# Optimization experiments

Hardware: AMD Instinct MI355X
Metric: run time of the kernel (lower is better)

Reference implementation:

```python
import jax, jax.numpy as jnp
import numpy as np

N_NODES = 50000
N_EDGES = 800000
D_FEAT = 128
D_HID = 128
N_CLASSES = 16


def setup_inputs() -> dict:
    key = jax.random.key(0)
    ks = jax.random.split(key, 5)
    x = jax.random.normal(ks[0], (N_NODES, D_FEAT), dtype=jnp.float32)
    edge_index = jax.random.randint(ks[1], (2, N_EDGES), 0, N_NODES, dtype=jnp.int32)
    # Glorot-ish scaled weights to keep activations in a sane range
    W1 = jax.random.normal(ks[2], (D_FEAT, D_HID), dtype=jnp.float32) * 0.05
    b1 = jnp.zeros((D_HID,), dtype=jnp.float32)
    W2 = jax.random.normal(ks[3], (D_HID, N_CLASSES), dtype=jnp.float32) * 0.05
    b2 = jnp.zeros((N_CLASSES,), dtype=jnp.float32)
    return {"x": x, "edge_index": edge_index, "W1": W1, "b1": b1, "W2": W2, "b2": b2}


def _gcn_conv(h, src, dst, norm, W, b, num_nodes):
    # linear transform first (F_in >= F_out ordering as in PyG GCNConv)
    h = h @ W                              # [N, F_out]
    msg = h[src] * norm[:, None]           # gather + edge-wise scale  [E+N, F_out]
    out = jax.ops.segment_sum(msg, dst, num_segments=num_nodes)  # scatter-add
    return out + b


def reference(x, edge_index, W1, b1, W2, b2):
    n = x.shape[0]
    loop = jnp.arange(n, dtype=edge_index.dtype)
    src = jnp.concatenate([edge_index[0], loop])  # add self-loops
    dst = jnp.concatenate([edge_index[1], loop])
    # symmetric normalization: deg^{-1/2}[src] * deg^{-1/2}[dst]
    deg = jax.ops.segment_sum(jnp.ones_like(dst, dtype=x.dtype), dst, num_segments=n)
    dis = jax.lax.rsqrt(jnp.maximum(deg, 1.0))  # deg >= 1 thanks to self-loops
    norm = dis[src] * dis[dst]
    h = jax.nn.relu(_gcn_conv(x, src, dst, norm, W1, b1, n))
    # dropout is identity in eval mode
    out = _gcn_conv(h, src, dst, norm, W2, b2, n)
    return jax.nn.sigmoid(out)
```

## Files before the change

### kernel.cpp

```cpp
#include <hip/hip_runtime.h>
#include <math.h>

#define NN 50000
#define NE 800000
#define DF 128
#define NC 16
#define WLD 136
#define NBIN 196
#define EPB 2048
#define HB ((NE + EPB - 1) / EPB)
#define HL (NBIN * HB)
#define PB ((HL + 255) / 256)
#define GB ((NN + 63) / 64)

typedef __bf16 bf16x8 __attribute__((ext_vector_type(8)));
typedef __bf16 bf16x4 __attribute__((ext_vector_type(4)));
typedef float  f32x4  __attribute__((ext_vector_type(4)));

__global__ void k_prep(const float* __restrict__ W1, const float* __restrict__ W2,
                       __bf16* __restrict__ W1T, __bf16* __restrict__ W2T) {
    int i = blockIdx.x * blockDim.x + threadIdx.x;
    if (i < DF * DF) {
        int n = i >> 7, k = i & 127;
        W1T[i] = (__bf16)W1[k * DF + n];
    }
    int j = i - DF * DF;
    if (j >= 0 && j < NC * DF) {
        int n = j >> 7, k = j & 127;
        W2T[j] = (__bf16)W2[k * NC + n];
    }
}

__global__ __launch_bounds__(256) void k_gemm1_hist(const float* __restrict__ X,
                                                    const __bf16* __restrict__ W1T,
                                                    __bf16* __restrict__ H1,
                                                    const int* __restrict__ dst,
                                                    int* __restrict__ h) {
    __shared__ __bf16 wlds[DF * WLD];
    __shared__ int hc[NBIN];
    if (blockIdx.x >= GB) {
        const int bb = blockIdx.x - GB;
        const int t = threadIdx.x;
        if (t < NBIN) hc[t] = 0;
        __syncthreads();
        const int base = bb * EPB;
#pragma unroll
        for (int i = 0; i < EPB / 256; ++i) {
            int e = base + i * 256 + t;
            if (e < NE) atomicAdd(&hc[dst[e] >> 8], 1);
        }
        __syncthreads();
        if (t < NBIN) h[t * HB + bb] = hc[t];
        return;
    }
    const int wid = threadIdx.x >> 6, lane = threadIdx.x & 63;
    const int m0 = blockIdx.x * 64 + wid * 16;
    const int m = m0 + (lane & 15);
    const int mc = (m < NN) ? m : NN - 1;
    const int l15 = lane & 15;
    const int kb = (lane >> 4) * 8;

    float4 xf[8];
#pragma unroll
    for (int q = 0; q < 4; ++q) {
        xf[2 * q]     = *(const float4*)&X[(size_t)mc * DF + q * 32 + kb];
        xf[2 * q + 1] = *(const float4*)&X[(size_t)mc * DF + q * 32 + kb + 4];
    }
    for (int i = threadIdx.x; i < DF * 16; i += 256) {
        int row = i >> 4, c8 = i & 15;
        *(bf16x8*)&wlds[row * WLD + c8 * 8] = ((const bf16x8*)W1T)[i];
    }
    __syncthreads();

    f32x4 acc[8];
#pragma unroll
    for (int nf = 0; nf < 8; ++nf) acc[nf] = (f32x4){0.f, 0.f, 0.f, 0.f};
#pragma unroll
    for (int ks = 0; ks < 4; ++ks) {
        float4 x0 = xf[2 * ks], x1 = xf[2 * ks + 1];
        bf16x8 xa;
        xa[0] = (__bf16)x0.x; xa[1] = (__bf16)x0.y; xa[2] = (__bf16)x0.z; xa[3] = (__bf16)x0.w;
        xa[4] = (__bf16)x1.x; xa[5] = (__bf16)x1.y; xa[6] = (__bf16)x1.z; xa[7] = (__bf16)x1.w;
#pragma unroll
        for (int nf = 0; nf < 8; ++nf) {
            bf16x8 wa = *(const bf16x8*)&wlds[(nf * 16 + l15) * WLD + ks * 32 + kb];
            acc[nf] = __builtin_amdgcn_mfma_f32_16x16x32_bf16(wa, xa, acc[nf], 0, 0, 0);
        }
    }
    if (m < NN) {
#pragma unroll
        for (int nf = 0; nf < 8; ++nf) {
            bf16x4 o;
            o[0] = (__bf16)acc[nf][0]; o[1] = (__bf16)acc[nf][1];
            o[2] = (__bf16)acc[nf][2]; o[3] = (__bf16)acc[nf][3];
            *(bf16x4*)&H1[(size_t)m * DF + nf * 16 + (lane >> 4) * 4] = o;
        }
    }
}

__global__ __launch_bounds__(256) void k_hpart(const int* __restrict__ h,
                                               int* __restrict__ part) {
    __shared__ int ws[4];
    const int b = blockIdx.x, t = threadIdx.x;
    const int idx = b * 256 + t;
    int s = (idx < HL) ? h[idx] : 0;
    for (int o = 32; o > 0; o >>= 1) s += __shfl_down(s, o);
    if ((t & 63) == 0) ws[t >> 6] = s;
    __syncthreads();
    if (t == 0) part[b] = ws[0] + ws[1] + ws[2] + ws[3];
}

__global__ __launch_bounds__(512) void k_hscan_part(const int* __restrict__ part,
                                                    int* __restrict__ partoff,
                                                    int* __restrict__ hscan) {
    __shared__ int s[512];
    const int t = threadIdx.x;
    int v = (t < PB) ? part[t] : 0;
    s[t] = v;
    __syncthreads();
    for (int o = 1; o < 512; o <<= 1) {
        int x = (t >= o) ? s[t - o] : 0;
        __syncthreads();
        s[t] += x;
        __syncthreads();
    }
    if (t < PB) partoff[t] = s[t] - v;
    if (t == 511) hscan[HL] = s[511];
}

__global__ __launch_bounds__(256) void k_hoff(const int* __restrict__ h,
                                              const int* __restrict__ partoff,
                                              int* __restrict__ hscan) {
    __shared__ int s[256];
    const int b = blockIdx.x, t = threadIdx.x;
    const int idx = b * 256 + t;
    int v = (idx < HL) ? h[idx] : 0;
    s[t] = v;
    __syncthreads();
    for (int o = 1; o < 256; o <<= 1) {
        int x = (t >= o) ? s[t - o] : 0;
        __syncthreads();
        s[t] += x;
        __syncthreads();
    }
    if (idx < HL) hscan[idx] = partoff[b] + s[t] - v;
}

__global__ __launch_bounds__(256) void k_scatterA(const int* __restrict__ src,
                                                  const int* __restrict__ dst,
                                                  const int* __restrict__ hscan,
                                                  int* __restrict__ ebuf) {
    __shared__ int cur[NBIN];
    const int bb = blockIdx.x, t = threadIdx.x;
    if (t < NBIN) cur[t] = hscan[t * HB + bb];
    __syncthreads();
    const int base = bb * EPB;
#pragma unroll
    for (int i = 0; i < EPB / 256; ++i) {
        int e = base + i * 256 + t;
        if (e < NE) {
            int s = src[e], d = dst[e];
            int pos = atomicAdd(&cur[d >> 8], 1);
            ebuf[pos] = s | ((d & 255) << 16);
        }
    }
}

__global__ __launch_bounds__(256) void k_rankB(const int* __restrict__ ebuf,
                                               const int* __restrict__ hscan,
                                               int* __restrict__ off,
                                               float* __restrict__ dis,
                                               unsigned short* __restrict__ rec) {
    __shared__ int cnt[256], s[256], cur[256];
    const int bin = blockIdx.x, t = threadIdx.x;
    const int base = hscan[bin * HB];
    const int end  = hscan[(bin + 1) * HB];
    cnt[t] = 0;
    __syncthreads();
    for (int e = base + t; e < end; e += 256)
        atomicAdd(&cnt[(ebuf[e] >> 16) & 255], 1);
    __syncthreads();
    int c = cnt[t];
    s[t] = c;
    __syncthreads();
    for (int o = 1; o < 256; o <<= 1) {
        int x = (t >= o) ? s[t - o] : 0;
        __syncthreads();
        s[t] += x;
        __syncthreads();
    }
    int lo = s[t] - c;
    int d = (bin << 8) + t;
    if (d < NN) {
        off[d] = base + lo;
        dis[d] = rsqrtf((float)(c + 1));
    }
    if (bin == NBIN - 1 && t == 0) off[NN] = NE;
    cur[t] = base + lo;
    __syncthreads();
    for (int e = base + t; e < end; e += 256) {
        int ed = ebuf[e];
        int p = atomicAdd(&cur[(ed >> 16) & 255], 1);
        rec[p] = (unsigned short)(ed & 0xFFFF);
    }
}

__global__ __launch_bounds__(256) void k_agg1g2(const __bf16* __restrict__ H1,
                                                const float* __restrict__ dis,
                                                const float* __restrict__ b1,
                                                const __bf16* __restrict__ W2T,
                                                const int* __restrict__ off,
                                                const unsigned short* __restrict__ rec,
                                                float* __restrict__ H2) {
    const int wid = threadIdx.x >> 6, lane = threadIdx.x & 63;
    const int n = blockIdx.x * 4 + wid;
    if (n >= NN) return;
    const int g = lane >> 4, l16 = lane & 15;
    const int fo = l16 * 8;
    const float dn = dis[n];

    float a[8];
#pragma unroll
    for (int i = 0; i < 8; ++i) a[i] = 0.f;

    const int e0 = off[n], e1 = off[n + 1];
    int e = e0 + g;
    for (; e + 12 < e1; e += 16) {
        int r0 = rec[e];
        int r1 = rec[e + 4];
        int r2 = rec[e + 8];
        int r3 = rec[e + 12];
        float w0 = dis[r0], w1 = dis[r1], w2 = dis[r2], w3 = dis[r3];
        bf16x8 h0 = *(const bf16x8*)&H1[(size_t)r0 * DF + fo];
        bf16x8 h1 = *(const bf16x8*)&H1[(size_t)r1 * DF + fo];
        bf16x8 h2 = *(const bf16x8*)&H1[(size_t)r2 * DF + fo];
        bf16x8 h3 = *(const bf16x8*)&H1[(size_t)r3 * DF + fo];
#pragma unroll
        for (int i = 0; i < 8; ++i) a[i] += (float)h0[i] * w0;
#pragma unroll
        for (int i = 0; i < 8; ++i) a[i] += (float)h1[i] * w1;
#pragma unroll
        for (int i = 0; i < 8; ++i) a[i] += (float)h2[i] * w2;
#pragma unroll
        for (int i = 0; i < 8; ++i) a[i] += (float)h3[i] * w3;
    }
    for (; e < e1; e += 4) {
        int r = rec[e];
        float w = dis[r];
        bf16x8 h = *(const bf16x8*)&H1[(size_t)r * DF + fo];
#pragma unroll
        for (int i = 0; i < 8; ++i) a[i] += (float)h[i] * w;
    }
#pragma unroll
    for (int i = 0; i < 8; ++i) {
        a[i] += __shfl_xor(a[i], 16);
        a[i] += __shfl_xor(a[i], 32);
    }
    {
        const float d2 = dn * dn;
        float4 b0 = *(const float4*)&b1[fo];
        float4 b4 = *(const float4*)&b1[fo + 4];
        bf16x8 hs = *(const bf16x8*)&H1[(size_t)n * DF + fo];
        a[0] = fmaxf(a[0] * dn + (float)hs[0] * d2 + b0.x, 0.f);
        a[1] = fmaxf(a[1] * dn + (float)hs[1] * d2 + b0.y, 0.f);
        a[2] = fmaxf(a[2] * dn + (float)hs[2] * d2 + b0.z, 0.f);
        a[3] = fmaxf(a[3] * dn + (float)hs[3] * d2 + b0.w, 0.f);
        a[4] = fmaxf(a[4] * dn + (float)hs[4] * d2 + b4.x, 0.f);
        a[5] = fmaxf(a[5] * dn + (float)hs[5] * d2 + b4.y, 0.f);
        a[6] = fmaxf(a[6] * dn + (float)hs[6] * d2 + b4.z, 0.f);
        a[7] = fmaxf(a[7] * dn + (float)hs[7] * d2 + b4.w, 0.f);
    }

    float p[4];
#pragma unroll
    for (int j = 0; j < 4; ++j) {
        bf16x8 wr = *(const bf16x8*)&W2T[(size_t)(g * 4 + j) * DF + fo];
        float s = 0.f;
#pragma unroll
        for (int i = 0; i < 8; ++i) s += a[i] * (float)wr[i];
        p[j] = s;
    }
#pragma unroll
    for (int o = 1; o <= 8; o <<= 1) {
#pragma unroll
        for (int j = 0; j < 4; ++j) p[j] += __shfl_xor(p[j], o);
    }
    if (l16 == 0) {
        f32x4 o4 = {p[0], p[1], p[2], p[3]};
        *(f32x4*)&H2[(size_t)n * NC + g * 4] = o4;
    }
}

__global__ __launch_bounds__(256) void k_agg2(const float* __restrict__ H2,
                                              const float* __restrict__ dis,
                                              const float* __restrict__ b2,
                                              const int* __restrict__ off,
                                              const unsigned short* __restrict__ rec,
                                              float* __restrict__ OUT) {
    const int wid = threadIdx.x >> 6, lane = threadIdx.x & 63;
    const int n = blockIdx.x * 4 + wid;
    if (n >= NN) return;
    const float dn = dis[n];

    const int g = lane >> 3, l8 = lane & 7;
    float ax = 0.f, ay = 0.f;
    const int e0 = off[n], e1 = off[n + 1];
    int e = e0 + g;
    for (; e + 8 < e1; e += 16) {
        int r0 = rec[e];
        int r1 = rec[e + 8];
        float w0 = dis[r0], w1 = dis[r1];
        float2 h0 = *(const float2*)&H2[(size_t)r0 * NC + l8 * 2];
        float2 h1 = *(const float2*)&H2[(size_t)r1 * NC + l8 * 2];
        ax += h0.x * w0;
        ay += h0.y * w0;
        ax += h1.x * w1;
        ay += h1.y * w1;
    }
    for (; e < e1; e += 8) {
        int r = rec[e];
        float w = dis[r];
        float2 h = *(const float2*)&H2[(size_t)r * NC + l8 * 2];
        ax += h.x * w;
        ay += h.y * w;
    }
    ax += __shfl_xor(ax, 8);  ay += __shfl_xor(ay, 8);
    ax += __shfl_xor(ax, 16); ay += __shfl_xor(ay, 16);
    ax += __shfl_xor(ax, 32); ay += __shfl_xor(ay, 32);
    if (g == 0) {
        float d2 = dn * dn;
        float2 hs = *(const float2*)&H2[(size_t)n * NC + l8 * 2];
        float2 bb = *(const float2*)&b2[l8 * 2];
        float vx = ax * dn + hs.x * d2 + bb.x;
        float vy = ay * dn + hs.y * d2 + bb.y;
        float2 o = { 1.0f / (1.0f + expf(-vx)), 1.0f / (1.0f + expf(-vy)) };
        *(float2*)&OUT[(size_t)n * NC + l8 * 2] = o;
    }
}

extern "C" void kernel_launch(void* const* d_in, const int* in_sizes, int n_in,
                              void* d_out, int out_size, void* d_ws, size_t ws_size,
                              hipStream_t stream) {
    const float* X  = (const float*)d_in[0];
    const int*   EI = (const int*)d_in[1];
    const float* W1 = (const float*)d_in[2];
    const float* b1 = (const float*)d_in[3];
    const float* W2 = (const float*)d_in[4];
    const float* b2 = (const float*)d_in[5];
    float* OUT = (float*)d_out;

    const int* src = EI;
    const int* dst = EI + NE;

    char* ws = (char*)d_ws;
    int*    h       = (int*)(ws);
    int*    hscan   = (int*)(ws + 327680);
    int*    hpart   = (int*)(ws + 655360);
    int*    hpartoff= (int*)(ws + 659456);
    int*    off     = (int*)(ws + 663552);
    float*  dis     = (float*)(ws + 868352);
    __bf16* W1T     = (__bf16*)(ws + 1073152);
    __bf16* W2T     = (__bf16*)(ws + 1105920);
    int*    ebuf    = (int*)(ws + 1110016);
    unsigned short* rec = (unsigned short*)(ws + 4310016);
    __bf16* H1      = (__bf16*)(ws + 5910016);
    float*  H2      = (float*)(ws + 18710016);

    const int B = 256;

    k_prep<<<(DF * DF + NC * DF + B - 1) / B, B, 0, stream>>>(W1, W2, W1T, W2T);
    k_gemm1_hist<<<GB + HB, B, 0, stream>>>(X, W1T, H1, dst, h);
    k_hpart<<<PB, B, 0, stream>>>(h, hpart);
    k_hscan_part<<<1, 512, 0, stream>>>(hpart, hpartoff, hscan);
    k_hoff<<<PB, B, 0, stream>>>(h, hpartoff, hscan);
    k_scatterA<<<HB, B, 0, stream>>>(src, dst, hscan, ebuf);
    k_rankB<<<NBIN, B, 0, stream>>>(ebuf, hscan, off, dis, rec);

    k_agg1g2<<<(NN + 3) / 4, B, 0, stream>>>(H1, dis, b1, W2T, off, rec, H2);
    k_agg2<<<(NN + 3) / 4, B, 0, stream>>>(H2, dis, b2, off, rec, OUT);
}
```

Measured before the change: 104.5 us.

## Slice H1 into feature-column slabs and split aggregation into sliced gather plus finalize

H1 is stored as 8 feature slabs of 16 columns each (1.6MB per slab), so the layer-1 gather runs one slab per block and its working set stays cache-resident. The fused agg1+GEMM2 kernel is split into k_aggS, which gathers and writes bf16 partial aggregates per slab, and k_fin, which applies the self-loop, bias, ReLU and W2 projection. The histogram edge-block size is also raised to shrink the scan. Each edge index is now read 8 times, and an extra intermediate buffer plus an extra launch are added.

Measured after the change: 195.6 us. 87.1% more time.

```diff
diff --git a/kernel.cpp b/kernel.cpp
--- a/kernel.cpp
+++ b/kernel.cpp
@@ -5,9 +5,11 @@
 #define NE 800000
 #define DF 128
 #define NC 16
+#define NSL 8
+#define SW 16
 #define WLD 136
 #define NBIN 196
-#define EPB 2048
+#define EPB 8192
 #define HB ((NE + EPB - 1) / EPB)
 #define HL (NBIN * HB)
 #define PB ((HL + 255) / 256)
@@ -33,7 +35,7 @@
 
 __global__ __launch_bounds__(256) void k_gemm1_hist(const float* __restrict__ X,
                                                     const __bf16* __restrict__ W1T,
-                                                    __bf16* __restrict__ H1,
+                                                    __bf16* __restrict__ H1s,
                                                     const int* __restrict__ dst,
                                                     int* __restrict__ h) {
     __shared__ __bf16 wlds[DF * WLD];
@@ -93,7 +95,7 @@
             bf16x4 o;
             o[0] = (__bf16)acc[nf][0]; o[1] = (__bf16)acc[nf][1];
             o[2] = (__bf16)acc[nf][2]; o[3] = (__bf16)acc[nf][3];
-            *(bf16x4*)&H1[(size_t)m * DF + nf * 16 + (lane >> 4) * 4] = o;
+            *(bf16x4*)&H1s[(size_t)nf * NN * SW + (size_t)m * SW + (lane >> 4) * 4] = o;
         }
     }
 }
@@ -110,22 +112,22 @@
     if (t == 0) part[b] = ws[0] + ws[1] + ws[2] + ws[3];
 }
 
-__global__ __launch_bounds__(512) void k_hscan_part(const int* __restrict__ part,
+__global__ __launch_bounds__(256) void k_hscan_part(const int* __restrict__ part,
                                                     int* __restrict__ partoff,
                                                     int* __restrict__ hscan) {
-    __shared__ int s[512];
+    __shared__ int s[256];
     const int t = threadIdx.x;
     int v = (t < PB) ? part[t] : 0;
     s[t] = v;
     __syncthreads();
-    for (int o = 1; o < 512; o <<= 1) {
+    for (int o = 1; o < 256; o <<= 1) {
         int x = (t >= o) ? s[t - o] : 0;
         __syncthreads();
         s[t] += x;
         __syncthreads();
     }
     if (t < PB) partoff[t] = s[t] - v;
-    if (t == 511) hscan[HL] = s[511];
+    if (t == 255) hscan[HL] = s[255];
 }
 
 __global__ __launch_bounds__(256) void k_hoff(const int* __restrict__ h,
@@ -205,80 +207,82 @@
     }
 }
 
-__global__ __launch_bounds__(256) void k_agg1g2(const __bf16* __restrict__ H1,
-                                                const float* __restrict__ dis,
-                                                const float* __restrict__ b1,
-                                                const __bf16* __restrict__ W2T,
-                                                const int* __restrict__ off,
-                                                const unsigned short* __restrict__ rec,
-                                                float* __restrict__ H2) {
+__global__ __launch_bounds__(256) void k_aggS(const __bf16* __restrict__ H1s,
+                                              const float* __restrict__ dis,
+                                              const int* __restrict__ off,
+                                              const unsigned short* __restrict__ rec,
+                                              __bf16* __restrict__ AGGs) {
+    const int s = blockIdx.x & (NSL - 1);
+    const int chunk = blockIdx.x >> 3;
+    const int wid = threadIdx.x >> 6, lane = threadIdx.x & 63;
+    const int n = chunk * 4 + wid;
+    const int eg = lane >> 2;
+    const int fl = lane & 3;
+    const __bf16* Hs = H1s + (size_t)s * NN * SW;
+
+    float a[4] = {0.f, 0.f, 0.f, 0.f};
+    const int e0 = off[n], e1 = off[n + 1];
+    for (int eb = e0; eb < e1; eb += 16) {
+        int e = eb + eg;
+        bool ok = e < e1;
+        int r = rec[ok ? e : eb];
+        float w = ok ? dis[r] : 0.f;
+        bf16x4 hv = *(const bf16x4*)&Hs[(size_t)r * SW + fl * 4];
+#pragma unroll
+        for (int i = 0; i < 4; ++i) a[i] += (float)hv[i] * w;
+    }
+#pragma unroll
+    for (int i = 0; i < 4; ++i) {
+        a[i] += __shfl_xor(a[i], 4);
+        a[i] += __shfl_xor(a[i], 8);
+        a[i] += __shfl_xor(a[i], 16);
+        a[i] += __shfl_xor(a[i], 32);
+    }
+    if (lane < 4) {
+        bf16x4 o;
+        o[0] = (__bf16)a[0]; o[1] = (__bf16)a[1];
+        o[2] = (__bf16)a[2]; o[3] = (__bf16)a[3];
+        *(bf16x4*)&AGGs[(size_t)s * NN * SW + (size_t)n * SW + fl * 4] = o;
+    }
+}
+
+__global__ __launch_bounds__(256) void k_fin(const __bf16* __restrict__ H1s,
+                                             const __bf16* __restrict__ AGGs,
+                                             const float* __restrict__ dis,
+                                             const float* __restrict__ b1,
+                                             const __bf16* __restrict__ W2T,
+                                             float* __restrict__ H2) {
     const int wid = threadIdx.x >> 6, lane = threadIdx.x & 63;
     const int n = blockIdx.x * 4 + wid;
     if (n >= NN) return;
     const int g = lane >> 4, l16 = lane & 15;
     const int fo = l16 * 8;
-    const float dn = dis[n];
+    const float dn = dis[n], d2 = dn * dn;
+    const size_t soff = (size_t)(l16 >> 1) * NN * SW + (size_t)n * SW + (l16 & 1) * 8;
+
+    bf16x8 ag = *(const bf16x8*)&AGGs[soff];
+    bf16x8 hs = *(const bf16x8*)&H1s[soff];
+    float4 b0 = *(const float4*)&b1[fo];
+    float4 b4 = *(const float4*)&b1[fo + 4];
 
     float a[8];
-#pragma unroll
-    for (int i = 0; i < 8; ++i) a[i] = 0.f;
-
-    const int e0 = off[n], e1 = off[n + 1];
-    int e = e0 + g;
-    for (; e + 12 < e1; e += 16) {
-        int r0 = rec[e];
-        int r1 = rec[e + 4];
-        int r2 = rec[e + 8];
-        int r3 = rec[e + 12];
-        float w0 = dis[r0], w1 = dis[r1], w2 = dis[r2], w3 = dis[r3];
-        bf16x8 h0 = *(const bf16x8*)&H1[(size_t)r0 * DF + fo];
-        bf16x8 h1 = *(const bf16x8*)&H1[(size_t)r1 * DF + fo];
-        bf16x8 h2 = *(const bf16x8*)&H1[(size_t)r2 * DF + fo];
-        bf16x8 h3 = *(const bf16x8*)&H1[(size_t)r3 * DF + fo];
-#pragma unroll
-        for (int i = 0; i < 8; ++i) a[i] += (float)h0[i] * w0;
-#pragma unroll
-        for (int i = 0; i < 8; ++i) a[i] += (float)h1[i] * w1;
-#pragma unroll
-        for (int i = 0; i < 8; ++i) a[i] += (float)h2[i] * w2;
-#pragma unroll
-        for (int i = 0; i < 8; ++i) a[i] += (float)h3[i] * w3;
-    }
-    for (; e < e1; e += 4) {
-        int r = rec[e];
-        float w = dis[r];
-        bf16x8 h = *(const bf16x8*)&H1[(size_t)r * DF + fo];
-#pragma unroll
-        for (int i = 0; i < 8; ++i) a[i] += (float)h[i] * w;
-    }
-#pragma unroll
-    for (int i = 0; i < 8; ++i) {
-        a[i] += __shfl_xor(a[i], 16);
-        a[i] += __shfl_xor(a[i], 32);
-    }
-    {
-        const float d2 = dn * dn;
-        float4 b0 = *(const float4*)&b1[fo];
-        float4 b4 = *(const float4*)&b1[fo + 4];
-        bf16x8 hs = *(const bf16x8*)&H1[(size_t)n * DF + fo];
-        a[0] = fmaxf(a[0] * dn + (float)hs[0] * d2 + b0.x, 0.f);
-        a[1] = fmaxf(a[1] * dn + (float)hs[1] * d2 + b0.y, 0.f);
-        a[2] = fmaxf(a[2] * dn + (float)hs[2] * d2 + b0.z, 0.f);
-        a[3] = fmaxf(a[3] * dn + (float)hs[3] * d2 + b0.w, 0.f);
-        a[4] = fmaxf(a[4] * dn + (float)hs[4] * d2 + b4.x, 0.f);
-        a[5] = fmaxf(a[5] * dn + (float)hs[5] * d2 + b4.y, 0.f);
-        a[6] = fmaxf(a[6] * dn + (float)hs[6] * d2 + b4.z, 0.f);
-        a[7] = fmaxf(a[7] * dn + (float)hs[7] * d2 + b4.w, 0.f);
-    }
+    a[0] = fmaxf((float)ag[0] * dn + (float)hs[0] * d2 + b0.x, 0.f);
+    a[1] = fmaxf((float)ag[1] * dn + (float)hs[1] * d2 + b0.y, 0.f);
+    a[2] = fmaxf((float)ag[2] * dn + (float)hs[2] * d2 + b0.z, 0.f);
+    a[3] = fmaxf((float)ag[3] * dn + (float)hs[3] * d2 + b0.w, 0.f);
+    a[4] = fmaxf((float)ag[4] * dn + (float)hs[4] * d2 + b4.x, 0.f);
+    a[5] = fmaxf((float)ag[5] * dn + (float)hs[5] * d2 + b4.y, 0.f);
+    a[6] = fmaxf((float)ag[6] * dn + (float)hs[6] * d2 + b4.z, 0.f);
+    a[7] = fmaxf((float)ag[7] * dn + (float)hs[7] * d2 + b4.w, 0.f);
 
     float p[4];
 #pragma unroll
     for (int j = 0; j < 4; ++j) {
         bf16x8 wr = *(const bf16x8*)&W2T[(size_t)(g * 4 + j) * DF + fo];
-        float s = 0.f;
-#pragma unroll
-        for (int i = 0; i < 8; ++i) s += a[i] * (float)wr[i];
-        p[j] = s;
+        float sum = 0.f;
+#pragma unroll
+        for (int i = 0; i < 8; ++i) sum += a[i] * (float)wr[i];
+        p[j] = sum;
     }
 #pragma unroll
     for (int o = 1; o <= 8; o <<= 1) {
@@ -354,28 +358,30 @@
 
     char* ws = (char*)d_ws;
     int*    h       = (int*)(ws);
-    int*    hscan   = (int*)(ws + 327680);
-    int*    hpart   = (int*)(ws + 655360);
-    int*    hpartoff= (int*)(ws + 659456);
-    int*    off     = (int*)(ws + 663552);
-    float*  dis     = (float*)(ws + 868352);
-    __bf16* W1T     = (__bf16*)(ws + 1073152);
-    __bf16* W2T     = (__bf16*)(ws + 1105920);
-    int*    ebuf    = (int*)(ws + 1110016);
-    unsigned short* rec = (unsigned short*)(ws + 4310016);
-    __bf16* H1      = (__bf16*)(ws + 5910016);
-    float*  H2      = (float*)(ws + 18710016);
+    int*    hscan   = (int*)(ws + 81920);
+    int*    hpart   = (int*)(ws + 163840);
+    int*    hpartoff= (int*)(ws + 167936);
+    int*    off     = (int*)(ws + 172032);
+    float*  dis     = (float*)(ws + 376832);
+    __bf16* W1T     = (__bf16*)(ws + 581632);
+    __bf16* W2T     = (__bf16*)(ws + 614400);
+    int*    ebuf    = (int*)(ws + 622592);
+    unsigned short* rec = (unsigned short*)(ws + 3822592);
+    __bf16* H1s     = (__bf16*)(ws + 5422592);
+    __bf16* AGGs    = (__bf16*)(ws + 18222592);
+    float*  H2      = (float*)(ws + 31022592);
 
     const int B = 256;
 
     k_prep<<<(DF * DF + NC * DF + B - 1) / B, B, 0, stream>>>(W1, W2, W1T, W2T);
-    k_gemm1_hist<<<GB + HB, B, 0, stream>>>(X, W1T, H1, dst, h);
+    k_gemm1_hist<<<GB + HB, B, 0, stream>>>(X, W1T, H1s, dst, h);
     k_hpart<<<PB, B, 0, stream>>>(h, hpart);
-    k_hscan_part<<<1, 512, 0, stream>>>(hpart, hpartoff, hscan);
+    k_hscan_part<<<1, B, 0, stream>>>(hpart, hpartoff, hscan);
     k_hoff<<<PB, B, 0, stream>>>(h, hpartoff, hscan);
     k_scatterA<<<HB, B, 0, stream>>>(src, dst, hscan, ebuf);
     k_rankB<<<NBIN, B, 0, stream>>>(ebuf, hscan, off, dis, rec);
 
-    k_agg1g2<<<(NN + 3) / 4, B, 0, stream>>>(H1, dis, b1, W2T, off, rec, H2);
+    k_aggS<<<NSL * (NN / 4), B, 0, stream>>>(H1s, dis, off, rec, AGGs);
+    k_fin<<<(NN + 3) / 4, B, 0, stream>>>(H1s, AGGs, dis, b1, W2T, H2);
     k_agg2<<<(NN + 3) / 4, B, 0, stream>>>(H2, dis, b2, off, rec, OUT);
 }
```

## Fuse GEMM1 with edge scatter, drop weight prep kernel, shrink bins

Applied to the files above, without the earlier changes.

Removes the separate weight-transpose kernel by having each GEMM block convert W1 to bf16 and transpose it into LDS itself, and by having agg1g2 read W2 directly in fp32. The GEMM is moved out of the histogram kernel and co-scheduled with the edge scatter pass. Histogram bins are narrowed to 128 nodes (391 bins) and edges per block raised to 8192, which shrinks the histogram/scan arrays and lets the scan run in one 256-thread block. In exchange, every GEMM block now does its own uncoalesced transposed LDS writes of W1 from fp32, and rankB leaves half its threads idle per bin.

New measurement: 138.1 us. 32.1% more time.

```diff
diff --git a/kernel.cpp b/kernel.cpp
--- a/kernel.cpp
+++ b/kernel.cpp
@@ -6,8 +6,8 @@
 #define DF 128
 #define NC 16
 #define WLD 136
-#define NBIN 196
-#define EPB 2048
+#define NBIN 391
+#define EPB 8192
 #define HB ((NE + EPB - 1) / EPB)
 #define HL (NBIN * HB)
 #define PB ((HL + 255) / 256)
@@ -17,85 +17,20 @@
 typedef __bf16 bf16x4 __attribute__((ext_vector_type(4)));
 typedef float  f32x4  __attribute__((ext_vector_type(4)));
 
-__global__ void k_prep(const float* __restrict__ W1, const float* __restrict__ W2,
-                       __bf16* __restrict__ W1T, __bf16* __restrict__ W2T) {
-    int i = blockIdx.x * blockDim.x + threadIdx.x;
-    if (i < DF * DF) {
-        int n = i >> 7, k = i & 127;
-        W1T[i] = (__bf16)W1[k * DF + n];
-    }
-    int j = i - DF * DF;
-    if (j >= 0 && j < NC * DF) {
-        int n = j >> 7, k = j & 127;
-        W2T[j] = (__bf16)W2[k * NC + n];
-    }
-}
-
-__global__ __launch_bounds__(256) void k_gemm1_hist(const float* __restrict__ X,
-                                                    const __bf16* __restrict__ W1T,
-                                                    __bf16* __restrict__ H1,
-                                                    const int* __restrict__ dst,
-                                                    int* __restrict__ h) {
-    __shared__ __bf16 wlds[DF * WLD];
+__global__ __launch_bounds__(256) void k_hist(const int* __restrict__ dst,
+                                              int* __restrict__ h) {
     __shared__ int hc[NBIN];
-    if (blockIdx.x >= GB) {
-        const int bb = blockIdx.x - GB;
-        const int t = threadIdx.x;
-        if (t < NBIN) hc[t] = 0;
-        __syncthreads();
-        const int base = bb * EPB;
-#pragma unroll
-        for (int i = 0; i < EPB / 256; ++i) {
-            int e = base + i * 256 + t;
-            if (e < NE) atomicAdd(&hc[dst[e] >> 8], 1);
-        }
-        __syncthreads();
-        if (t < NBIN) h[t * HB + bb] = hc[t];
-        return;
-    }
-    const int wid = threadIdx.x >> 6, lane = threadIdx.x & 63;
-    const int m0 = blockIdx.x * 64 + wid * 16;
-    const int m = m0 + (lane & 15);
-    const int mc = (m < NN) ? m : NN - 1;
-    const int l15 = lane & 15;
-    const int kb = (lane >> 4) * 8;
-
-    float4 xf[8];
-#pragma unroll
-    for (int q = 0; q < 4; ++q) {
-        xf[2 * q]     = *(const float4*)&X[(size_t)mc * DF + q * 32 + kb];
-        xf[2 * q + 1] = *(const float4*)&X[(size_t)mc * DF + q * 32 + kb + 4];
-    }
-    for (int i = threadIdx.x; i < DF * 16; i += 256) {
-        int row = i >> 4, c8 = i & 15;
-        *(bf16x8*)&wlds[row * WLD + c8 * 8] = ((const bf16x8*)W1T)[i];
-    }
-    __syncthreads();
-
-    f32x4 acc[8];
-#pragma unroll
-    for (int nf = 0; nf < 8; ++nf) acc[nf] = (f32x4){0.f, 0.f, 0.f, 0.f};
-#pragma unroll
-    for (int ks = 0; ks < 4; ++ks) {
-        float4 x0 = xf[2 * ks], x1 = xf[2 * ks + 1];
-        bf16x8 xa;
-        xa[0] = (__bf16)x0.x; xa[1] = (__bf16)x0.y; xa[2] = (__bf16)x0.z; xa[3] = (__bf16)x0.w;
-        xa[4] = (__bf16)x1.x; xa[5] = (__bf16)x1.y; xa[6] = (__bf16)x1.z; xa[7] = (__bf16)x1.w;
-#pragma unroll
-        for (int nf = 0; nf < 8; ++nf) {
-            bf16x8 wa = *(const bf16x8*)&wlds[(nf * 16 + l15) * WLD + ks * 32 + kb];
-            acc[nf] = __builtin_amdgcn_mfma_f32_16x16x32_bf16(wa, xa, acc[nf], 0, 0, 0);
-        }
-    }
-    if (m < NN) {
-#pragma unroll
-        for (int nf = 0; nf < 8; ++nf) {
-            bf16x4 o;
-            o[0] = (__bf16)acc[nf][0]; o[1] = (__bf16)acc[nf][1];
-            o[2] = (__bf16)acc[nf][2]; o[3] = (__bf16)acc[nf][3];
-            *(bf16x4*)&H1[(size_t)m * DF + nf * 16 + (lane >> 4) * 4] = o;
-        }
-    }
+    const int bb = blockIdx.x, t = threadIdx.x;
+    for (int i = t; i < NBIN; i += 256) hc[i] = 0;
+    __syncthreads();
+    const int base = bb * EPB;
+#pragma unroll
+    for (int i = 0; i < EPB / 256; ++i) {
+        int e = base + i * 256 + t;
+        if (e < NE) atomicAdd(&hc[dst[e] >> 7], 1);
+    }
+    __syncthreads();
+    for (int i = t; i < NBIN; i += 256) h[i * HB + bb] = hc[i];
 }
 
 __global__ __launch_bounds__(256) void k_hpart(const int* __restrict__ h,
@@ -110,22 +45,22 @@
     if (t == 0) part[b] = ws[0] + ws[1] + ws[2] + ws[3];
 }
 
-__global__ __launch_bounds__(512) void k_hscan_part(const int* __restrict__ part,
+__global__ __launch_bounds__(256) void k_hscan_part(const int* __restrict__ part,
                                                     int* __restrict__ partoff,
                                                     int* __restrict__ hscan) {
-    __shared__ int s[512];
+    __shared__ int s[256];
     const int t = threadIdx.x;
     int v = (t < PB) ? part[t] : 0;
     s[t] = v;
     __syncthreads();
-    for (int o = 1; o < 512; o <<= 1) {
+    for (int o = 1; o < 256; o <<= 1) {
         int x = (t >= o) ? s[t - o] : 0;
         __syncthreads();
         s[t] += x;
         __syncthreads();
     }
     if (t < PB) partoff[t] = s[t] - v;
-    if (t == 511) hscan[HL] = s[511];
+    if (t == 255) hscan[HL] = s[255];
 }
 
 __global__ __launch_bounds__(256) void k_hoff(const int* __restrict__ h,
@@ -146,22 +81,73 @@
     if (idx < HL) hscan[idx] = partoff[b] + s[t] - v;
 }
 
-__global__ __launch_bounds__(256) void k_scatterA(const int* __restrict__ src,
-                                                  const int* __restrict__ dst,
-                                                  const int* __restrict__ hscan,
-                                                  int* __restrict__ ebuf) {
+__global__ __launch_bounds__(256) void k_gemm1_scatter(const float* __restrict__ X,
+                                                       const float* __restrict__ W1,
+                                                       __bf16* __restrict__ H1,
+                                                       const int* __restrict__ src,
+                                                       const int* __restrict__ dst,
+                                                       const int* __restrict__ hscan,
+                                                       int* __restrict__ ebuf) {
+    __shared__ __bf16 wlds[DF * WLD];
     __shared__ int cur[NBIN];
-    const int bb = blockIdx.x, t = threadIdx.x;
-    if (t < NBIN) cur[t] = hscan[t * HB + bb];
-    __syncthreads();
-    const int base = bb * EPB;
-#pragma unroll
-    for (int i = 0; i < EPB / 256; ++i) {
-        int e = base + i * 256 + t;
-        if (e < NE) {
-            int s = src[e], d = dst[e];
-            int pos = atomicAdd(&cur[d >> 8], 1);
-            ebuf[pos] = s | ((d & 255) << 16);
+    if (blockIdx.x >= GB) {
+        const int bb = blockIdx.x - GB;
+        const int t = threadIdx.x;
+        for (int i = t; i < NBIN; i += 256) cur[i] = hscan[i * HB + bb];
+        __syncthreads();
+        const int base = bb * EPB;
+#pragma unroll
+        for (int i = 0; i < EPB / 256; ++i) {
+            int e = base + i * 256 + t;
+            if (e < NE) {
+                int s = src[e], d = dst[e];
+                int pos = atomicAdd(&cur[d >> 7], 1);
+                ebuf[pos] = s | ((d & 127) << 16);
+            }
+        }
+        return;
+    }
+    const int wid = threadIdx.x >> 6, lane = threadIdx.x & 63;
+    const int m0 = blockIdx.x * 64 + wid * 16;
+    const int m = m0 + (lane & 15);
+    const int mc = (m < NN) ? m : NN - 1;
+    const int l15 = lane & 15;
+    const int kb = (lane >> 4) * 8;
+
+    float4 xf[8];
+#pragma unroll
+    for (int q = 0; q < 4; ++q) {
+        xf[2 * q]     = *(const float4*)&X[(size_t)mc * DF + q * 32 + kb];
+        xf[2 * q + 1] = *(const float4*)&X[(size_t)mc * DF + q * 32 + kb + 4];
+    }
+    for (int i = threadIdx.x; i < DF * DF; i += 256) {
+        int k = i >> 7, n = i & 127;
+        wlds[n * WLD + k] = (__bf16)W1[i];
+    }
+    __syncthreads();
+
+    f32x4 acc[8];
+#pragma unroll
+    for (int nf = 0; nf < 8; ++nf) acc[nf] = (f32x4){0.f, 0.f, 0.f, 0.f};
+#pragma unroll
+    for (int ks = 0; ks < 4; ++ks) {
+        float4 x0 = xf[2 * ks], x1 = xf[2 * ks + 1];
+        bf16x8 xa;
+        xa[0] = (__bf16)x0.x; xa[1] = (__bf16)x0.y; xa[2] = (__bf16)x0.z; xa[3] = (__bf16)x0.w;
+        xa[4] = (__bf16)x1.x; xa[5] = (__bf16)x1.y; xa[6] = (__bf16)x1.z; xa[7] = (__bf16)x1.w;
+#pragma unroll
+        for (int nf = 0; nf < 8; ++nf) {
+            bf16x8 wa = *(const bf16x8*)&wlds[(nf * 16 + l15) * WLD + ks * 32 + kb];
+            acc[nf] = __builtin_amdgcn_mfma_f32_16x16x32_bf16(wa, xa, acc[nf], 0, 0, 0);
+        }
+    }
+    if (m < NN) {
+#pragma unroll
+        for (int nf = 0; nf < 8; ++nf) {
+            bf16x4 o;
+            o[0] = (__bf16)acc[nf][0]; o[1] = (__bf16)acc[nf][1];
+            o[2] = (__bf16)acc[nf][2]; o[3] = (__bf16)acc[nf][3];
+            *(bf16x4*)&H1[(size_t)m * DF + nf * 16 + (lane >> 4) * 4] = o;
         }
     }
 }
@@ -171,16 +157,16 @@
                                                int* __restrict__ off,
                                                float* __restrict__ dis,
                                                unsigned short* __restrict__ rec) {
-    __shared__ int cnt[256], s[256], cur[256];
+    __shared__ int cnt[128], s[256], cur[128];
     const int bin = blockIdx.x, t = threadIdx.x;
     const int base = hscan[bin * HB];
     const int end  = hscan[(bin + 1) * HB];
-    cnt[t] = 0;
+    if (t < 128) cnt[t] = 0;
     __syncthreads();
     for (int e = base + t; e < end; e += 256)
-        atomicAdd(&cnt[(ebuf[e] >> 16) & 255], 1);
-    __syncthreads();
-    int c = cnt[t];
+        atomicAdd(&cnt[(ebuf[e] >> 16) & 127], 1);
+    __syncthreads();
+    int c = (t < 128) ? cnt[t] : 0;
     s[t] = c;
     __syncthreads();
     for (int o = 1; o < 256; o <<= 1) {
@@ -190,17 +176,17 @@
         __syncthreads();
     }
     int lo = s[t] - c;
-    int d = (bin << 8) + t;
-    if (d < NN) {
+    int d = (bin << 7) + t;
+    if (t < 128 && d < NN) {
         off[d] = base + lo;
         dis[d] = rsqrtf((float)(c + 1));
     }
     if (bin == NBIN - 1 && t == 0) off[NN] = NE;
-    cur[t] = base + lo;
+    if (t < 128) cur[t] = base + lo;
     __syncthreads();
     for (int e = base + t; e < end; e += 256) {
         int ed = ebuf[e];
-        int p = atomicAdd(&cur[(ed >> 16) & 255], 1);
+        int p = atomicAdd(&cur[(ed >> 16) & 127], 1);
         rec[p] = (unsigned short)(ed & 0xFFFF);
     }
 }
@@ -208,7 +194,7 @@
 __global__ __launch_bounds__(256) void k_agg1g2(const __bf16* __restrict__ H1,
                                                 const float* __restrict__ dis,
                                                 const float* __restrict__ b1,
-                                                const __bf16* __restrict__ W2T,
+                                                const float* __restrict__ W2,
                                                 const int* __restrict__ off,
                                                 const unsigned short* __restrict__ rec,
                                                 float* __restrict__ H2) {
@@ -271,14 +257,14 @@
         a[7] = fmaxf(a[7] * dn + (float)hs[7] * d2 + b4.w, 0.f);
     }
 
-    float p[4];
-#pragma unroll
-    for (int j = 0; j < 4; ++j) {
-        bf16x8 wr = *(const bf16x8*)&W2T[(size_t)(g * 4 + j) * DF + fo];
-        float s = 0.f;
-#pragma unroll
-        for (int i = 0; i < 8; ++i) s += a[i] * (float)wr[i];
-        p[j] = s;
+    float p[4] = {0.f, 0.f, 0.f, 0.f};
+#pragma unroll
+    for (int i = 0; i < 8; ++i) {
+        float4 wv = *(const float4*)&W2[(size_t)(fo + i) * NC + g * 4];
+        p[0] += a[i] * wv.x;
+        p[1] += a[i] * wv.y;
+        p[2] += a[i] * wv.z;
+        p[3] += a[i] * wv.w;
     }
 #pragma unroll
     for (int o = 1; o <= 8; o <<= 1) {
@@ -354,28 +340,25 @@
 
     char* ws = (char*)d_ws;
     int*    h       = (int*)(ws);
-    int*    hscan   = (int*)(ws + 327680);
-    int*    hpart   = (int*)(ws + 655360);
-    int*    hpartoff= (int*)(ws + 659456);
-    int*    off     = (int*)(ws + 663552);
-    float*  dis     = (float*)(ws + 868352);
-    __bf16* W1T     = (__bf16*)(ws + 1073152);
-    __bf16* W2T     = (__bf16*)(ws + 1105920);
-    int*    ebuf    = (int*)(ws + 1110016);
-    unsigned short* rec = (unsigned short*)(ws + 4310016);
-    __bf16* H1      = (__bf16*)(ws + 5910016);
-    float*  H2      = (float*)(ws + 18710016);
+    int*    hscan   = (int*)(ws + 163840);
+    int*    hpart   = (int*)(ws + 327680);
+    int*    hpartoff= (int*)(ws + 331776);
+    int*    off     = (int*)(ws + 335872);
+    float*  dis     = (float*)(ws + 540672);
+    int*    ebuf    = (int*)(ws + 745472);
+    unsigned short* rec = (unsigned short*)(ws + 3945472);
+    __bf16* H1      = (__bf16*)(ws + 5545472);
+    float*  H2      = (float*)(ws + 18345472);
 
     const int B = 256;
 
-    k_prep<<<(DF * DF + NC * DF + B - 1) / B, B, 0, stream>>>(W1, W2, W1T, W2T);
-    k_gemm1_hist<<<GB + HB, B, 0, stream>>>(X, W1T, H1, dst, h);
+    k_hist<<<HB, B, 0, stream>>>(dst, h);
     k_hpart<<<PB, B, 0, stream>>>(h, hpart);
-    k_hscan_part<<<1, 512, 0, stream>>>(hpart, hpartoff, hscan);
+    k_hscan_part<<<1, B, 0, stream>>>(hpart, hpartoff, hscan);
     k_hoff<<<PB, B, 0, stream>>>(h, hpartoff, hscan);
-    k_scatterA<<<HB, B, 0, stream>>>(src, dst, hscan, ebuf);
+    k_gemm1_scatter<<<GB + HB, B, 0, stream>>>(X, W1, H1, src, dst, hscan, ebuf);
     k_rankB<<<NBIN, B, 0, stream>>>(ebuf, hscan, off, dis, rec);
 
-    k_agg1g2<<<(NN + 3) / 4, B, 0, stream>>>(H1, dis, b1, W2T, off, rec, H2);
+    k_agg1g2<<<(NN + 3) / 4, B, 0, stream>>>(H1, dis, b1, W2, off, rec, H2);
     k_agg2<<<(NN + 3) / 4, B, 0, stream>>>(H2, dis, b2, off, rec, OUT);
 }
```
